# Kernel optimization log

Measured on AMD Instinct MI355X. Metric: run time of the kernel, lower is better.

The kernel has to match this reference:

```python
import jax, jax.numpy as jnp
import numpy as np


def setup_inputs() -> dict:
    key = jax.random.key(0)
    k0, k1, k2, k3, k4, k5 = jax.random.split(key, 6)
    B, S, D = 8, 4096, 1024
    x = jax.random.normal(k0, (B, S, D), dtype=jnp.float32)
    labels = jax.random.randint(k1, (B, S), 0, 2, dtype=jnp.int32)
    mask = jnp.ones((B, S), dtype=bool)  # torchcrf requires mask[:, 0] all on
    W = jax.random.normal(k2, (2, D), dtype=jnp.float32) / np.float32(np.sqrt(D))
    b = jnp.zeros((2,), dtype=jnp.float32)
    start_transitions = jax.random.uniform(k3, (2,), jnp.float32, -0.1, 0.1)
    end_transitions = jax.random.uniform(k4, (2,), jnp.float32, -0.1, 0.1)
    transitions = jax.random.uniform(k5, (2, 2), jnp.float32, -0.1, 0.1)
    return {"x": x, "labels": labels, "mask": mask, "W": W, "b": b,
            "start_transitions": start_transitions,
            "end_transitions": end_transitions,
            "transitions": transitions}


def _crf_neg_log_likelihood(logits, labels, mask, start_transitions, end_transitions, transitions):
    # torchcrf CRF(num_tags=2, batch_first=True), reduction='sum'
    maskf = mask.astype(logits.dtype)  # (B, S)
    # ---- numerator: score of the gold tag sequence ----
    emit = jnp.take_along_axis(logits, labels[..., None], axis=2)[..., 0]  # (B, S)
    num = start_transitions[labels[:, 0]] + emit[:, 0]
    num = num + jnp.sum(emit[:, 1:] * maskf[:, 1:], axis=1)
    num = num + jnp.sum(transitions[labels[:, :-1], labels[:, 1:]] * maskf[:, 1:], axis=1)
    seq_ends = jnp.sum(mask.astype(jnp.int32), axis=1) - 1  # (B,)
    last_tags = jnp.take_along_axis(labels, seq_ends[:, None], axis=1)[:, 0]
    num = num + end_transitions[last_tags]
    # ---- denominator: forward algorithm (log partition) via scan over time ----
    def step(alpha, inp):
        e, m = inp  # e: (B, 2) emissions at t, m: (B,) mask at t
        nxt = jax.nn.logsumexp(alpha[:, :, None] + transitions[None, :, :] + e[:, None, :], axis=1)
        alpha = jnp.where(m[:, None], nxt, alpha)
        return alpha, None
    alpha0 = start_transitions[None, :] + logits[:, 0]  # (B, 2)
    emis_t = jnp.swapaxes(logits, 0, 1)[1:]  # (S-1, B, 2)
    mask_t = jnp.swapaxes(mask, 0, 1)[1:]    # (S-1, B)
    alpha, _ = jax.lax.scan(step, alpha0, (emis_t, mask_t))
    logZ = jax.nn.logsumexp(alpha + end_transitions[None, :], axis=1)  # (B,)
    llh = jnp.sum(num - logZ)  # reduction='sum'
    return -llh


def reference(x, labels, mask, W, b, start_transitions, end_transitions, transitions):
    # dropout is identity at inference
    logits = jnp.einsum('bsd,td->bst', x, W) + b  # (B, S, 2)
    neg_llh = _crf_neg_log_likelihood(logits, labels, mask,
                                      start_transitions, end_transitions, transitions)
    # module returns (-loss, logits) where loss = crf(...) = log-likelihood sum
    return (neg_llh, logits)
```

## Files before the change

kernel.cpp:

```cpp
#include <hip/hip_runtime.h>
#include <math.h>

#define NB 8
#define S  4096
#define D  1024
#define RPW 4
#define NWAVES (NB * S / RPW)

__device__ inline float lse2(float a, float b) {
    float m = fmaxf(a, b);
    float d = fminf(a, b) - m;
    return m + __logf(1.f + __expf(d));
}

__global__ __launch_bounds__(256, 4) void logits_kernel(
    const float* __restrict__ x, const float* __restrict__ W,
    const float* __restrict__ b, const int* __restrict__ labels,
    const float* __restrict__ trans,
    float* __restrict__ out,
    float4* __restrict__ wsP,
    float* __restrict__ wsN)
{
    int wave = (blockIdx.x * blockDim.x + threadIdx.x) >> 6;
    int lane = threadIdx.x & 63;
    int row0 = wave * RPW;
    int s0   = row0 & (S - 1);
    int batch = row0 >> 12;

    float4 w0[4], w1[4];
#pragma unroll
    for (int k = 0; k < 4; ++k) {
        int c = (lane + 64 * k) * 4;
        w0[k] = *(const float4*)(W + c);
        w1[k] = *(const float4*)(W + D + c);
    }
    float b0 = b[0], b1 = b[1];
    float tr00 = trans[0], tr01 = trans[1], tr10 = trans[2], tr11 = trans[3];

    const int* labp = labels + batch * S + s0;
    int lm1 = (s0 > 0) ? labp[-1] : 0;
    int l0 = labp[0], l1 = labp[1], l2 = labp[2], l3 = labp[3];

    float2 ee[4];
#pragma unroll
    for (int r = 0; r < RPW; ++r) {
        const float* xr = x + (size_t)(row0 + r) * D;
        float4 xv[4];
#pragma unroll
        for (int k = 0; k < 4; ++k) xv[k] = *(const float4*)(xr + (lane + 64 * k) * 4);
        float a0 = 0.f, a1 = 0.f;
#pragma unroll
        for (int k = 0; k < 4; ++k) {
            a0 += xv[k].x*w0[k].x + xv[k].y*w0[k].y + xv[k].z*w0[k].z + xv[k].w*w0[k].w;
            a1 += xv[k].x*w1[k].x + xv[k].y*w1[k].y + xv[k].z*w1[k].z + xv[k].w*w1[k].w;
        }
#pragma unroll
        for (int off = 32; off >= 1; off >>= 1) {
            a0 += __shfl_xor(a0, off, 64);
            a1 += __shfl_xor(a1, off, 64);
        }
        ee[r].x = a0 + b0;
        ee[r].y = a1 + b1;
        if (lane == 0) {
            size_t o = 1 + (size_t)(row0 + r) * 2;
            out[o]     = ee[r].x;
            out[o + 1] = ee[r].y;
        }
    }

    auto trsel = [&](int i, int j) {
        return j ? (i ? tr11 : tr01) : (i ? tr10 : tr00);
    };
    float num = (l0 ? ee[0].y : ee[0].x)
              + (l1 ? ee[1].y : ee[1].x)
              + (l2 ? ee[2].y : ee[2].x)
              + (l3 ? ee[3].y : ee[3].x);
    num += trsel(l0, l1) + trsel(l1, l2) + trsel(l2, l3);
    if (s0 > 0) num += trsel(lm1, l0);

    float P00, P01, P10, P11;
    auto comb = [&](float2 e) {
        float M00 = tr00 + e.x, M01 = tr01 + e.y, M10 = tr10 + e.x, M11 = tr11 + e.y;
        float n00 = lse2(P00 + M00, P01 + M10);
        float n01 = lse2(P00 + M01, P01 + M11);
        float n10 = lse2(P10 + M00, P11 + M10);
        float n11 = lse2(P10 + M01, P11 + M11);
        P00 = n00; P01 = n01; P10 = n10; P11 = n11;
    };
    if (s0 == 0) {
        P00 = tr00 + ee[1].x; P01 = tr01 + ee[1].y;
        P10 = tr10 + ee[1].x; P11 = tr11 + ee[1].y;
        comb(ee[2]); comb(ee[3]);
    } else {
        P00 = tr00 + ee[0].x; P01 = tr01 + ee[0].y;
        P10 = tr10 + ee[0].x; P11 = tr11 + ee[0].y;
        comb(ee[1]); comb(ee[2]); comb(ee[3]);
    }

    if (lane == 0) {
        wsP[wave] = make_float4(P00, P01, P10, P11);
        wsN[wave] = num;
    }
    if (blockIdx.x == 0 && threadIdx.x == 0) out[0] = 0.f;
}

__global__ __launch_bounds__(256) void crf_reduce_kernel(
    const float* __restrict__ out_logits, const int* __restrict__ labels,
    const float* __restrict__ start_t, const float* __restrict__ end_t,
    const float4* __restrict__ wsP, const float* __restrict__ wsN,
    float* __restrict__ result)
{
    const int bidx = blockIdx.x;
    const int t = threadIdx.x;
    const int wbase = bidx * (S / RPW) + t * 4;

    float4 A = wsP[wbase];
    float num = wsN[wbase];
#pragma unroll
    for (int k = 1; k < 4; ++k) {
        float4 Bm = wsP[wbase + k];
        num += wsN[wbase + k];
        float4 R;
        R.x = lse2(A.x + Bm.x, A.y + Bm.z);
        R.y = lse2(A.x + Bm.y, A.y + Bm.w);
        R.z = lse2(A.z + Bm.x, A.w + Bm.z);
        R.w = lse2(A.z + Bm.y, A.w + Bm.w);
        A = R;
    }

    __shared__ float4 Ps[256];
    __shared__ float red[256];
    Ps[t] = A; red[t] = num;
    __syncthreads();
    for (int off = 1; off < 256; off <<= 1) {
        if ((t & (2 * off - 1)) == 0) {
            float4 Aa = Ps[t], Bb = Ps[t + off];
            float4 R;
            R.x = lse2(Aa.x + Bb.x, Aa.y + Bb.z);
            R.y = lse2(Aa.x + Bb.y, Aa.y + Bb.w);
            R.z = lse2(Aa.z + Bb.x, Aa.w + Bb.z);
            R.w = lse2(Aa.z + Bb.y, Aa.w + Bb.w);
            Ps[t] = R;
            red[t] += red[t + off];
        }
        __syncthreads();
    }

    if (t == 0) {
        const float* lg  = out_logits + 1 + (size_t)bidx * S * 2;
        const int*   lab = labels + (size_t)bidx * S;
        float4 P = Ps[0];
        float a0 = start_t[0] + lg[0];
        float a1 = start_t[1] + lg[1];
        float f0 = lse2(a0 + P.x, a1 + P.z);
        float f1 = lse2(a0 + P.y, a1 + P.w);
        float logZ = lse2(f0 + end_t[0], f1 + end_t[1]);
        float numt = red[0] + start_t[lab[0]] + end_t[lab[S - 1]];
        atomicAdd(result, logZ - numt);
    }
}

extern "C" void kernel_launch(void* const* d_in, const int* in_sizes, int n_in,
                              void* d_out, int out_size, void* d_ws, size_t ws_size,
                              hipStream_t stream) {
    const float* x      = (const float*)d_in[0];
    const int*   labels = (const int*)  d_in[1];
    const float* W      = (const float*)d_in[3];
    const float* b      = (const float*)d_in[4];
    const float* st     = (const float*)d_in[5];
    const float* et     = (const float*)d_in[6];
    const float* tr     = (const float*)d_in[7];
    float* out = (float*)d_out;

    float4* wsP = (float4*)d_ws;
    float*  wsN = (float*)((char*)d_ws + (size_t)NWAVES * sizeof(float4));

    const int waves  = NB * S / RPW;
    const int blocks = waves / 4;
    logits_kernel<<<blocks, 256, 0, stream>>>(x, W, b, labels, tr, out, wsP, wsN);
    crf_reduce_kernel<<<NB, 256, 0, stream>>>(out, labels, st, et, wsP, wsN, out);
}
```

Before: 214.4 us.

## Process 16 rows per wave with double-buffered loads and batched shuffle reductions

Measured after the change: 231.3 us. 7.9% more time.

```diff
diff --git a/kernel.cpp b/kernel.cpp
--- a/kernel.cpp
+++ b/kernel.cpp
@@ -4,8 +4,9 @@
 #define NB 8
 #define S  4096
 #define D  1024
-#define RPW 4
+#define RPW 16
 #define NWAVES (NB * S / RPW)
+#define PPB (S / RPW)
 
 __device__ inline float lse2(float a, float b) {
     float m = fmaxf(a, b);
@@ -13,7 +14,7 @@
     return m + __logf(1.f + __expf(d));
 }
 
-__global__ __launch_bounds__(256, 4) void logits_kernel(
+__global__ __launch_bounds__(256, 2) void logits_kernel(
     const float* __restrict__ x, const float* __restrict__ W,
     const float* __restrict__ b, const int* __restrict__ labels,
     const float* __restrict__ trans,
@@ -21,11 +22,11 @@
     float4* __restrict__ wsP,
     float* __restrict__ wsN)
 {
-    int wave = (blockIdx.x * blockDim.x + threadIdx.x) >> 6;
-    int lane = threadIdx.x & 63;
-    int row0 = wave * RPW;
-    int s0   = row0 & (S - 1);
-    int batch = row0 >> 12;
+    const int wave = (blockIdx.x * blockDim.x + threadIdx.x) >> 6;
+    const int lane = threadIdx.x & 63;
+    const int row0 = wave * RPW;
+    const int s0   = row0 & (S - 1);
+    const int batch = row0 >> 12;
 
     float4 w0[4], w1[4];
 #pragma unroll
@@ -34,49 +35,57 @@
         w0[k] = *(const float4*)(W + c);
         w1[k] = *(const float4*)(W + D + c);
     }
-    float b0 = b[0], b1 = b[1];
-    float tr00 = trans[0], tr01 = trans[1], tr10 = trans[2], tr11 = trans[3];
+    const float b0 = b[0], b1 = b[1];
+    const float tr00 = trans[0], tr01 = trans[1], tr10 = trans[2], tr11 = trans[3];
 
     const int* labp = labels + batch * S + s0;
-    int lm1 = (s0 > 0) ? labp[-1] : 0;
-    int l0 = labp[0], l1 = labp[1], l2 = labp[2], l3 = labp[3];
-
-    float2 ee[4];
-#pragma unroll
-    for (int r = 0; r < RPW; ++r) {
-        const float* xr = x + (size_t)(row0 + r) * D;
-        float4 xv[4];
-#pragma unroll
-        for (int k = 0; k < 4; ++k) xv[k] = *(const float4*)(xr + (lane + 64 * k) * 4);
-        float a0 = 0.f, a1 = 0.f;
-#pragma unroll
-        for (int k = 0; k < 4; ++k) {
-            a0 += xv[k].x*w0[k].x + xv[k].y*w0[k].y + xv[k].z*w0[k].z + xv[k].w*w0[k].w;
-            a1 += xv[k].x*w1[k].x + xv[k].y*w1[k].y + xv[k].z*w1[k].z + xv[k].w*w1[k].w;
+    int4 lv[4];
+#pragma unroll
+    for (int q = 0; q < 4; ++q) lv[q] = ((const int4*)labp)[q];
+    const int lm1 = (s0 > 0) ? labp[-1] : 0;
+
+    const float* xbase = x + (size_t)row0 * D;
+
+    auto LOADG = [&](float4 (&buf)[4][4], int g) {
+#pragma unroll
+        for (int r = 0; r < 4; ++r)
+#pragma unroll
+            for (int k = 0; k < 4; ++k)
+                buf[r][k] = *(const float4*)(xbase + (size_t)(g * 4 + r) * D + (lane + 64 * k) * 4);
+    };
+
+    auto COMPG = [&](const float4 (&buf)[4][4], int g, float2 (&ee)[4]) {
+        float a[4], c[4];
+#pragma unroll
+        for (int r = 0; r < 4; ++r) {
+            float sa = 0.f, sc = 0.f;
+#pragma unroll
+            for (int k = 0; k < 4; ++k) {
+                sa += buf[r][k].x*w0[k].x + buf[r][k].y*w0[k].y + buf[r][k].z*w0[k].z + buf[r][k].w*w0[k].w;
+                sc += buf[r][k].x*w1[k].x + buf[r][k].y*w1[k].y + buf[r][k].z*w1[k].z + buf[r][k].w*w1[k].w;
+            }
+            a[r] = sa; c[r] = sc;
         }
 #pragma unroll
         for (int off = 32; off >= 1; off >>= 1) {
-            a0 += __shfl_xor(a0, off, 64);
-            a1 += __shfl_xor(a1, off, 64);
-        }
-        ee[r].x = a0 + b0;
-        ee[r].y = a1 + b1;
+#pragma unroll
+            for (int r = 0; r < 4; ++r) {
+                a[r] += __shfl_xor(a[r], off, 64);
+                c[r] += __shfl_xor(c[r], off, 64);
+            }
+        }
+#pragma unroll
+        for (int r = 0; r < 4; ++r) { ee[r].x = a[r] + b0; ee[r].y = c[r] + b1; }
         if (lane == 0) {
-            size_t o = 1 + (size_t)(row0 + r) * 2;
-            out[o]     = ee[r].x;
-            out[o + 1] = ee[r].y;
-        }
-    }
+            size_t o = 1 + (size_t)(row0 + g * 4) * 2;
+#pragma unroll
+            for (int r = 0; r < 4; ++r) { out[o + 2*r] = ee[r].x; out[o + 2*r + 1] = ee[r].y; }
+        }
+    };
 
     auto trsel = [&](int i, int j) {
         return j ? (i ? tr11 : tr01) : (i ? tr10 : tr00);
     };
-    float num = (l0 ? ee[0].y : ee[0].x)
-              + (l1 ? ee[1].y : ee[1].x)
-              + (l2 ? ee[2].y : ee[2].x)
-              + (l3 ? ee[3].y : ee[3].x);
-    num += trsel(l0, l1) + trsel(l1, l2) + trsel(l2, l3);
-    if (s0 > 0) num += trsel(lm1, l0);
 
     float P00, P01, P10, P11;
     auto comb = [&](float2 e) {
@@ -87,14 +96,59 @@
         float n11 = lse2(P10 + M01, P11 + M11);
         P00 = n00; P01 = n01; P10 = n10; P11 = n11;
     };
-    if (s0 == 0) {
-        P00 = tr00 + ee[1].x; P01 = tr01 + ee[1].y;
-        P10 = tr10 + ee[1].x; P11 = tr11 + ee[1].y;
-        comb(ee[2]); comb(ee[3]);
-    } else {
-        P00 = tr00 + ee[0].x; P01 = tr01 + ee[0].y;
-        P10 = tr10 + ee[0].x; P11 = tr11 + ee[0].y;
-        comb(ee[1]); comb(ee[2]); comb(ee[3]);
+
+    float4 bufA[4][4], bufB[4][4];
+    float2 ee[4];
+    float num = 0.f;
+
+    LOADG(bufA, 0);
+    LOADG(bufB, 1);
+
+    COMPG(bufA, 0, ee);
+    {
+        int l0 = lv[0].x, l1 = lv[0].y, l2 = lv[0].z, l3 = lv[0].w;
+        num += (l0 ? ee[0].y : ee[0].x) + (l1 ? ee[1].y : ee[1].x)
+             + (l2 ? ee[2].y : ee[2].x) + (l3 ? ee[3].y : ee[3].x);
+        num += trsel(l0, l1) + trsel(l1, l2) + trsel(l2, l3);
+        if (s0 > 0) num += trsel(lm1, l0);
+        if (s0 == 0) {
+            P00 = tr00 + ee[1].x; P01 = tr01 + ee[1].y;
+            P10 = tr10 + ee[1].x; P11 = tr11 + ee[1].y;
+            comb(ee[2]); comb(ee[3]);
+        } else {
+            P00 = tr00 + ee[0].x; P01 = tr01 + ee[0].y;
+            P10 = tr10 + ee[0].x; P11 = tr11 + ee[0].y;
+            comb(ee[1]); comb(ee[2]); comb(ee[3]);
+        }
+    }
+    LOADG(bufA, 2);
+
+    COMPG(bufB, 1, ee);
+    {
+        int lp = lv[0].w, l0 = lv[1].x, l1 = lv[1].y, l2 = lv[1].z, l3 = lv[1].w;
+        num += (l0 ? ee[0].y : ee[0].x) + (l1 ? ee[1].y : ee[1].x)
+             + (l2 ? ee[2].y : ee[2].x) + (l3 ? ee[3].y : ee[3].x);
+        num += trsel(lp, l0) + trsel(l0, l1) + trsel(l1, l2) + trsel(l2, l3);
+        comb(ee[0]); comb(ee[1]); comb(ee[2]); comb(ee[3]);
+    }
+    LOADG(bufB, 3);
+
+    COMPG(bufA, 2, ee);
+    {
+        int lp = lv[1].w, l0 = lv[2].x, l1 = lv[2].y, l2 = lv[2].z, l3 = lv[2].w;
+        num += (l0 ? ee[0].y : ee[0].x) + (l1 ? ee[1].y : ee[1].x)
+             + (l2 ? ee[2].y : ee[2].x) + (l3 ? ee[3].y : ee[3].x);
+        num += trsel(lp, l0) + trsel(l0, l1) + trsel(l1, l2) + trsel(l2, l3);
+        comb(ee[0]); comb(ee[1]); comb(ee[2]); comb(ee[3]);
+    }
+
+    COMPG(bufB, 3, ee);
+    {
+        int lp = lv[2].w, l0 = lv[3].x, l1 = lv[3].y, l2 = lv[3].z, l3 = lv[3].w;
+        num += (l0 ? ee[0].y : ee[0].x) + (l1 ? ee[1].y : ee[1].x)
+             + (l2 ? ee[2].y : ee[2].x) + (l3 ? ee[3].y : ee[3].x);
+        num += trsel(lp, l0) + trsel(l0, l1) + trsel(l1, l2) + trsel(l2, l3);
+        comb(ee[0]); comb(ee[1]); comb(ee[2]); comb(ee[3]);
     }
 
     if (lane == 0) {
@@ -112,21 +166,10 @@
 {
     const int bidx = blockIdx.x;
     const int t = threadIdx.x;
-    const int wbase = bidx * (S / RPW) + t * 4;
+    const int wbase = bidx * PPB + t;
 
     float4 A = wsP[wbase];
     float num = wsN[wbase];
-#pragma unroll
-    for (int k = 1; k < 4; ++k) {
-        float4 Bm = wsP[wbase + k];
-        num += wsN[wbase + k];
-        float4 R;
-        R.x = lse2(A.x + Bm.x, A.y + Bm.z);
-        R.y = lse2(A.x + Bm.y, A.y + Bm.w);
-        R.z = lse2(A.z + Bm.x, A.w + Bm.z);
-        R.w = lse2(A.z + Bm.y, A.w + Bm.w);
-        A = R;
-    }
 
     __shared__ float4 Ps[256];
     __shared__ float red[256];
```
